# Optimization experiments

Hardware: AMD Instinct MI355X
Metric: run time of the kernel (lower is better)

## Reference

```python
import jax, jax.numpy as jnp
import numpy as np

HEAD = 16  # from init_kwargs
NEG_FILL = -1e20


def setup_inputs() -> dict:
    key = jax.random.key(0)
    ks = jax.random.split(key, 6)
    N, S, E = 4, 2048, 1024
    D = E // HEAD  # 64
    value = jax.random.normal(ks[0], (N, S, E), dtype=jnp.float32)
    key_t = jax.random.normal(ks[1], (N, S, E), dtype=jnp.float32)
    query = jax.random.normal(ks[2], (N, S, E), dtype=jnp.float32)
    # multiplicative causal mask broadcastable to (N, H, S, S)
    mask = jnp.tril(jnp.ones((S, S), dtype=jnp.float32))[None, None, :, :]
    # per-head-dim projection weights (Dense(head_dim) applied after reshape,
    # so weights are (D, D), shared across heads) -- faithful to source
    sc = 1.0 / np.sqrt(D)
    Wq = jax.random.normal(ks[3], (D, D), dtype=jnp.float32) * sc
    Wk = jax.random.normal(ks[4], (D, D), dtype=jnp.float32) * sc
    Wv = jax.random.normal(ks[5], (D, D), dtype=jnp.float32) * sc
    return {"value": value, "key": key_t, "query": query, "mask": mask,
            "Wq": Wq, "Wk": Wk, "Wv": Wv}


def reference(value, key, query, mask, Wq, Wk, Wv):
    N, Lq, E = query.shape
    H = HEAD
    D = E // H
    # reshape to heads, then project last dim (D -> D)
    q = jnp.einsum('nqhd,de->nqhe', query.reshape(N, Lq, H, D), Wq)
    k = jnp.einsum('nkhd,de->nkhe', key.reshape(N, key.shape[1], H, D), Wk)
    v = jnp.einsum('nvhd,de->nvhe', value.reshape(N, value.shape[1], H, D), Wv)
    # unscaled QK^T (source has no 1/sqrt(d))
    energy = jnp.einsum('nqhd,nkhd->nhqk', q, k)  # (N,H,Lq,Lk)
    energy = energy * mask
    energy = jnp.where(energy == 0, NEG_FILL, energy)
    attention = jax.nn.softmax(energy, axis=-1)
    out = jnp.einsum('nhql,nlhd->nqhd', attention, v).reshape(N, Lq, H * D)
    return out  # fc_layer defined in __init__ but never used in call()
```

## Files before the change

kernel.cpp:

```cpp
#include <hip/hip_runtime.h>
#include <hip/hip_bf16.h>
#include <math.h>


#define NB  4
#define SEQ 2048
#define HD  16
#define DH  64
#define NH  (NB*HD)

typedef _Float16 half8  __attribute__((ext_vector_type(8)));
typedef _Float16 half2  __attribute__((ext_vector_type(2)));
typedef __fp16   fp16x2 __attribute__((ext_vector_type(2)));
typedef float    f32x4  __attribute__((ext_vector_type(4)));
typedef float    f32x16 __attribute__((ext_vector_type(16)));

__device__ inline half2 pkrtz(float a, float b) {
  union { fp16x2 f; half2 h; } u;
  u.f = __builtin_amdgcn_cvt_pkrtz(a, b);
  return u.h;
}

__device__ inline void gload16(const void* g, void* l) {
  __builtin_amdgcn_global_load_lds(
      (const __attribute__((address_space(1))) void*)g,
      (__attribute__((address_space(3))) void*)l, 16, 0, 0);
}

__global__ __launch_bounds__(256) void proj_kernel(
    const float* __restrict__ q_in, const float* __restrict__ k_in,
    const float* __restrict__ v_in,
    const float* __restrict__ Wq, const float* __restrict__ Wk,
    const float* __restrict__ Wv,
    _Float16* __restrict__ Qp, _Float16* __restrict__ Kp,
    _Float16* __restrict__ Vt)
{
  __shared__ float Wl[64*64];
  const int t = threadIdx.x;
  const int which = blockIdx.z;
  const float* in = which == 0 ? q_in : (which == 1 ? k_in : v_in);
  const float* W  = which == 0 ? Wq   : (which == 1 ? Wk   : Wv);

  const int nh = blockIdx.y;
  const int n = nh >> 4, h = nh & 15;
  const int s0 = blockIdx.x * 256;

  #pragma unroll
  for (int i = 0; i < 16; ++i) Wl[i*256 + t] = W[i*256 + t];
  __syncthreads();

  const int w = t >> 6, lane = t & 63, lr = lane & 15, lg = lane >> 4;

  if (which < 2) {
    half8 bfr[4][2];
    #pragma unroll
    for (int g = 0; g < 4; ++g)
      #pragma unroll
      for (int kc = 0; kc < 2; ++kc)
        #pragma unroll
        for (int i = 0; i < 8; ++i)
          bfr[g][kc][i] = (_Float16)Wl[(kc*32 + lg*8 + i)*64 + 16*g + lr];

    _Float16* outp = (which == 0 ? Qp : Kp) + (size_t)nh*SEQ*DH;
    #pragma unroll
    for (int pass = 0; pass < 4; ++pass) {
      int row0 = s0 + (pass*4 + w)*16;
      const float* ip = in + ((size_t)(n*SEQ + row0 + lr))*(HD*DH) + h*DH;
      float4 a0 = *(const float4*)(ip + lg*8);
      float4 a1 = *(const float4*)(ip + lg*8 + 4);
      float4 a2 = *(const float4*)(ip + 32 + lg*8);
      float4 a3 = *(const float4*)(ip + 32 + lg*8 + 4);
      half8 af0, af1;
      af0[0]=(_Float16)a0.x; af0[1]=(_Float16)a0.y; af0[2]=(_Float16)a0.z; af0[3]=(_Float16)a0.w;
      af0[4]=(_Float16)a1.x; af0[5]=(_Float16)a1.y; af0[6]=(_Float16)a1.z; af0[7]=(_Float16)a1.w;
      af1[0]=(_Float16)a2.x; af1[1]=(_Float16)a2.y; af1[2]=(_Float16)a2.z; af1[3]=(_Float16)a2.w;
      af1[4]=(_Float16)a3.x; af1[5]=(_Float16)a3.y; af1[6]=(_Float16)a3.z; af1[7]=(_Float16)a3.w;
      f32x4 c[4] = {{0,0,0,0},{0,0,0,0},{0,0,0,0},{0,0,0,0}};
      #pragma unroll
      for (int g = 0; g < 4; ++g) {
        c[g] = __builtin_amdgcn_mfma_f32_16x16x32_f16(af0, bfr[g][0], c[g], 0, 0, 0);
        c[g] = __builtin_amdgcn_mfma_f32_16x16x32_f16(af1, bfr[g][1], c[g], 0, 0, 0);
      }
      #pragma unroll
      for (int g = 0; g < 4; ++g)
        #pragma unroll
        for (int j = 0; j < 4; ++j)
          outp[(size_t)(row0 + 4*lg + j)*DH + 16*g + lr] = (_Float16)c[g][j];
    }
  } else {
    half8 afr[2];
    #pragma unroll
    for (int kc = 0; kc < 2; ++kc)
      #pragma unroll
      for (int i = 0; i < 8; ++i)
        afr[kc][i] = (_Float16)Wl[(kc*32 + lg*8 + i)*64 + w*16 + lr];

    _Float16* outp = Vt + (size_t)nh*DH*SEQ;
    #pragma unroll
    for (int pass = 0; pass < 4; ++pass) {
      int sc0 = s0 + pass*64;
      f32x4 c[4] = {{0,0,0,0},{0,0,0,0},{0,0,0,0},{0,0,0,0}};
      #pragma unroll
      for (int g = 0; g < 4; ++g) {
        const float* ip = in + ((size_t)(n*SEQ + sc0 + 16*g + lr))*(HD*DH) + h*DH;
        float4 b0 = *(const float4*)(ip + lg*8);
        float4 b1 = *(const float4*)(ip + lg*8 + 4);
        float4 b2 = *(const float4*)(ip + 32 + lg*8);
        float4 b3 = *(const float4*)(ip + 32 + lg*8 + 4);
        half8 bf0, bf1;
        bf0[0]=(_Float16)b0.x; bf0[1]=(_Float16)b0.y; bf0[2]=(_Float16)b0.z; bf0[3]=(_Float16)b0.w;
        bf0[4]=(_Float16)b1.x; bf0[5]=(_Float16)b1.y; bf0[6]=(_Float16)b1.z; bf0[7]=(_Float16)b1.w;
        bf1[0]=(_Float16)b2.x; bf1[1]=(_Float16)b2.y; bf1[2]=(_Float16)b2.z; bf1[3]=(_Float16)b2.w;
        bf1[4]=(_Float16)b3.x; bf1[5]=(_Float16)b3.y; bf1[6]=(_Float16)b3.z; bf1[7]=(_Float16)b3.w;
        c[g] = __builtin_amdgcn_mfma_f32_16x16x32_f16(afr[0], bf0, c[g], 0, 0, 0);
        c[g] = __builtin_amdgcn_mfma_f32_16x16x32_f16(afr[1], bf1, c[g], 0, 0, 0);
      }
      #pragma unroll
      for (int g = 0; g < 4; ++g)
        #pragma unroll
        for (int j = 0; j < 4; ++j) {
          int kcol = 16*g + lr;
          int pcol = (kcol & ~12) | ((kcol & 8) >> 1) | ((kcol & 4) << 1);
          outp[(size_t)(w*16 + 4*lg + j)*SEQ + sc0 + pcol] = (_Float16)c[g][j];
        }
    }
  }
}

__global__ __launch_bounds__(256) void attn_kernel(
    const _Float16* __restrict__ Qp,
    const _Float16* __restrict__ Kp,
    const _Float16* __restrict__ Vt,
    float* __restrict__ out)
{
  __shared__ __attribute__((aligned(16))) _Float16 Kl[2][64*64];
  __shared__ __attribute__((aligned(16))) _Float16 Vl[2][64*64];

  const int nh = blockIdx.y;
  const int n = nh >> 4, h = nh & 15;
  const int sb = ((blockIdx.y >> 4) & 1) ? (int)blockIdx.x : (15 - (int)blockIdx.x);
  const int qs = sb * 128;
  const int tid = threadIdx.x;
  const int w = tid >> 6, lane = tid & 63;
  const int lq = lane & 31, lg1 = lane >> 5;
  const int q0 = qs + w*32;
  const int q  = q0 + lq;

  const _Float16* Kbase = Kp + (size_t)nh*SEQ*DH;
  const _Float16* Vbase = Vt + (size_t)nh*DH*SEQ;

  const _Float16* Qrow = Qp + ((size_t)nh*SEQ + q)*DH + 8*lg1;
  half8 qf[4];
  #pragma unroll
  for (int c = 0; c < 4; ++c) qf[c] = *(const half8*)(Qrow + 16*c);

  int roff[2][4];
  #pragma unroll
  for (int rt = 0; rt < 2; ++rt)
    #pragma unroll
    for (int c = 0; c < 4; ++c)
      roff[rt][c] = (32*rt + lq)*128 + (((2*c + lg1) ^ (lq & 7)) << 4);

  const int srow = tid >> 3;
  const int scs  = (tid & 7) ^ (srow & 7);
  const _Float16* kg = Kbase + (size_t)srow*DH + scs*8;
  const _Float16* vg = Vbase + (size_t)srow*SEQ + scs*8;

  float m = -INFINITY, lsum = 0.f;
  f32x16 o0 = {0,0,0,0,0,0,0,0,0,0,0,0,0,0,0,0};
  f32x16 o1 = {0,0,0,0,0,0,0,0,0,0,0,0,0,0,0,0};

  const int Tw   = q0 >> 6;
  const int Tmax = 2*sb + 1;

  gload16(kg,            &Kl[0][tid*8]);
  gload16(kg + 32*DH,    &Kl[0][(256+tid)*8]);
  gload16(vg,            &Vl[0][tid*8]);
  gload16(vg + 32*SEQ,   &Vl[0][(256+tid)*8]);

  int cur = 0;
  for (int t = 0; t <= Tmax; ++t) {
    if (t < Tmax) {
      const _Float16* kgt = kg + (size_t)(t+1)*64*DH;
      const _Float16* vgt = vg + (t+1)*64;
      _Float16* kd = &Kl[cur^1][0];
      _Float16* vd = &Vl[cur^1][0];
      gload16(kgt,          kd + tid*8);
      gload16(kgt + 32*DH,  kd + (256+tid)*8);
      gload16(vgt,          vd + tid*8);
      gload16(vgt + 32*SEQ, vd + (256+tid)*8);
      asm volatile("s_waitcnt vmcnt(4)" ::: "memory");
    } else {
      asm volatile("s_waitcnt vmcnt(0)" ::: "memory");
    }
    __builtin_amdgcn_sched_barrier(0);
    __builtin_amdgcn_s_barrier();
    __builtin_amdgcn_sched_barrier(0);

    if (t <= Tw) {
      const char* Kb = (const char*)&Kl[cur][0];
      const char* Vb = (const char*)&Vl[cur][0];
      const int kt = t*64;

      f32x16 s0 = {0,0,0,0,0,0,0,0,0,0,0,0,0,0,0,0};
      f32x16 s1 = {0,0,0,0,0,0,0,0,0,0,0,0,0,0,0,0};
      #pragma unroll
      for (int c = 0; c < 4; ++c) {
        half8 ka = *(const half8*)(Kb + roff[0][c]);
        half8 kb = *(const half8*)(Kb + roff[1][c]);
        s0 = __builtin_amdgcn_mfma_f32_32x32x16_f16(ka, qf[c], s0, 0, 0, 0);
        s1 = __builtin_amdgcn_mfma_f32_32x32x16_f16(kb, qf[c], s1, 0, 0, 0);
      }
      if (t == Tw) {
        #pragma unroll
        for (int j = 0; j < 16; ++j) {
          int kl = 4*lg1 + 8*(j>>2) + (j&3);
          if (kt + kl      > q) s0[j] = -1e30f;
          if (kt + 32 + kl > q) s1[j] = -1e30f;
        }
      }
      float t0[8];
      #pragma unroll
      for (int j = 0; j < 8; ++j)
        t0[j] = fmaxf(fmaxf(s0[j], s0[j+8]), fmaxf(s1[j], s1[j+8]));
      float pm = fmaxf(fmaxf(fmaxf(t0[0],t0[1]), fmaxf(t0[2],t0[3])),
                       fmaxf(fmaxf(t0[4],t0[5]), fmaxf(t0[6],t0[7])));
      pm = fmaxf(pm, __shfl_xor(pm, 32));
      float mn = fmaxf(m, pm);
      float sc = __expf(m - mn);
      m = mn;
      #pragma unroll
      for (int j = 0; j < 16; ++j) {
        s0[j] = __expf(s0[j] - m);
        s1[j] = __expf(s1[j] - m);
      }
      float u0[8];
      #pragma unroll
      for (int j = 0; j < 8; ++j)
        u0[j] = (s0[j] + s0[j+8]) + (s1[j] + s1[j+8]);
      float ps = ((u0[0]+u0[1]) + (u0[2]+u0[3])) + ((u0[4]+u0[5]) + (u0[6]+u0[7]));
      ps += __shfl_xor(ps, 32);
      lsum = lsum*sc + ps;
      #pragma unroll
      for (int j = 0; j < 16; ++j) { o0[j] *= sc; o1[j] *= sc; }

      half2 pkA[8], pkB[8];
      #pragma unroll
      for (int jj = 0; jj < 8; ++jj) {
        pkA[jj] = pkrtz(s0[2*jj], s0[2*jj+1]);
        pkB[jj] = pkrtz(s1[2*jj], s1[2*jj+1]);
      }
      #pragma unroll
      for (int c = 0; c < 4; ++c) {
        union { half8 h; half2 p[4]; } pb;
        pb.p[0] = (c < 2) ? pkA[(c&1)*4 + 0] : pkB[(c&1)*4 + 0];
        pb.p[1] = (c < 2) ? pkA[(c&1)*4 + 1] : pkB[(c&1)*4 + 1];
        pb.p[2] = (c < 2) ? pkA[(c&1)*4 + 2] : pkB[(c&1)*4 + 2];
        pb.p[3] = (c < 2) ? pkA[(c&1)*4 + 3] : pkB[(c&1)*4 + 3];
        half8 va = *(const half8*)(Vb + roff[0][c]);
        half8 vb = *(const half8*)(Vb + roff[1][c]);
        o0 = __builtin_amdgcn_mfma_f32_32x32x16_f16(va, pb.h, o0, 0, 0, 0);
        o1 = __builtin_amdgcn_mfma_f32_32x32x16_f16(vb, pb.h, o1, 0, 0, 0);
      }
    }

    __builtin_amdgcn_sched_barrier(0);
    __builtin_amdgcn_s_barrier();
    cur ^= 1;
  }

  float inv = 1.0f / lsum;
  float* orow = out + ((size_t)n*SEQ + q)*(HD*DH) + h*DH;
  #pragma unroll
  for (int j = 0; j < 16; ++j) {
    int dl = 4*lg1 + 8*(j>>2) + (j&3);
    orow[dl]      = o0[j] * inv;
    orow[32 + dl] = o1[j] * inv;
  }
}

extern "C" void kernel_launch(void* const* d_in, const int* in_sizes, int n_in,
                              void* d_out, int out_size, void* d_ws, size_t ws_size,
                              hipStream_t stream) {
  (void)in_sizes; (void)n_in; (void)out_size; (void)ws_size;
  const float* value = (const float*)d_in[0];
  const float* key   = (const float*)d_in[1];
  const float* query = (const float*)d_in[2];
  const float* Wq = (const float*)d_in[4];
  const float* Wk = (const float*)d_in[5];
  const float* Wv = (const float*)d_in[6];

  _Float16* Qp = (_Float16*)d_ws;
  _Float16* Kp = Qp + (size_t)NH*SEQ*DH;
  _Float16* Vt = Kp + (size_t)NH*SEQ*DH;
  float* out = (float*)d_out;

  proj_kernel<<<dim3(8, 64, 3), 256, 0, stream>>>(query, key, value,
                                                  Wq, Wk, Wv, Qp, Kp, Vt);
  attn_kernel<<<dim3(16, 64), 256, 0, stream>>>(Qp, Kp, Vt, out);
}
```

Measured before the change: 127.5 us.

## Use single-wave attention blocks with direct global K/V loads, exp2 and lazy rescale

```diff
diff --git a/kernel.cpp b/kernel.cpp
--- a/kernel.cpp
+++ b/kernel.cpp
@@ -19,12 +19,6 @@
   union { fp16x2 f; half2 h; } u;
   u.f = __builtin_amdgcn_cvt_pkrtz(a, b);
   return u.h;
-}
-
-__device__ inline void gload16(const void* g, void* l) {
-  __builtin_amdgcn_global_load_lds(
-      (const __attribute__((address_space(1))) void*)g,
-      (__attribute__((address_space(3))) void*)l, 16, 0, 0);
 }
 
 __global__ __launch_bounds__(256) void proj_kernel(
@@ -52,6 +46,7 @@
   const int w = t >> 6, lane = t & 63, lr = lane & 15, lg = lane >> 4;
 
   if (which < 2) {
+    const float oscale = (which == 0) ? 1.44269504088896f : 1.0f;
     half8 bfr[4][2];
     #pragma unroll
     for (int g = 0; g < 4; ++g)
@@ -85,7 +80,8 @@
       for (int g = 0; g < 4; ++g)
         #pragma unroll
         for (int j = 0; j < 4; ++j)
-          outp[(size_t)(row0 + 4*lg + j)*DH + 16*g + lr] = (_Float16)c[g][j];
+          outp[(size_t)(row0 + 4*lg + j)*DH + 16*g + lr] =
+              (_Float16)(c[g][j] * oscale);
     }
   } else {
     half8 afr[2];
@@ -127,146 +123,102 @@
   }
 }
 
-__global__ __launch_bounds__(256) void attn_kernel(
+__global__ __launch_bounds__(64) void attn_kernel(
     const _Float16* __restrict__ Qp,
     const _Float16* __restrict__ Kp,
     const _Float16* __restrict__ Vt,
     float* __restrict__ out)
 {
-  __shared__ __attribute__((aligned(16))) _Float16 Kl[2][64*64];
-  __shared__ __attribute__((aligned(16))) _Float16 Vl[2][64*64];
-
-  const int nh = blockIdx.y;
-  const int n = nh >> 4, h = nh & 15;
-  const int sb = ((blockIdx.y >> 4) & 1) ? (int)blockIdx.x : (15 - (int)blockIdx.x);
-  const int qs = sb * 128;
-  const int tid = threadIdx.x;
-  const int w = tid >> 6, lane = tid & 63;
+  const int bid  = blockIdx.x;
+  const int head = bid & 63;
+  const int q32  = bid >> 6;
+  const int n = head >> 4, h = head & 15;
+  const int lane = threadIdx.x;
   const int lq = lane & 31, lg1 = lane >> 5;
-  const int q0 = qs + w*32;
+  const int q0 = q32 * 32;
   const int q  = q0 + lq;
-
-  const _Float16* Kbase = Kp + (size_t)nh*SEQ*DH;
-  const _Float16* Vbase = Vt + (size_t)nh*DH*SEQ;
-
-  const _Float16* Qrow = Qp + ((size_t)nh*SEQ + q)*DH + 8*lg1;
+  const int Tmax = q32 >> 1;
+
+  const _Float16* Kbase = Kp + (size_t)head*SEQ*DH;
+  const _Float16* Vbase = Vt + (size_t)head*DH*SEQ;
+
+  const _Float16* Qrow = Qp + ((size_t)head*SEQ + q)*DH + 8*lg1;
   half8 qf[4];
   #pragma unroll
   for (int c = 0; c < 4; ++c) qf[c] = *(const half8*)(Qrow + 16*c);
 
-  int roff[2][4];
-  #pragma unroll
-  for (int rt = 0; rt < 2; ++rt)
-    #pragma unroll
-    for (int c = 0; c < 4; ++c)
-      roff[rt][c] = (32*rt + lq)*128 + (((2*c + lg1) ^ (lq & 7)) << 4);
-
-  const int srow = tid >> 3;
-  const int scs  = (tid & 7) ^ (srow & 7);
-  const _Float16* kg = Kbase + (size_t)srow*DH + scs*8;
-  const _Float16* vg = Vbase + (size_t)srow*SEQ + scs*8;
-
   float m = -INFINITY, lsum = 0.f;
   f32x16 o0 = {0,0,0,0,0,0,0,0,0,0,0,0,0,0,0,0};
   f32x16 o1 = {0,0,0,0,0,0,0,0,0,0,0,0,0,0,0,0};
 
-  const int Tw   = q0 >> 6;
-  const int Tmax = 2*sb + 1;
-
-  gload16(kg,            &Kl[0][tid*8]);
-  gload16(kg + 32*DH,    &Kl[0][(256+tid)*8]);
-  gload16(vg,            &Vl[0][tid*8]);
-  gload16(vg + 32*SEQ,   &Vl[0][(256+tid)*8]);
-
-  int cur = 0;
   for (int t = 0; t <= Tmax; ++t) {
-    if (t < Tmax) {
-      const _Float16* kgt = kg + (size_t)(t+1)*64*DH;
-      const _Float16* vgt = vg + (t+1)*64;
-      _Float16* kd = &Kl[cur^1][0];
-      _Float16* vd = &Vl[cur^1][0];
-      gload16(kgt,          kd + tid*8);
-      gload16(kgt + 32*DH,  kd + (256+tid)*8);
-      gload16(vgt,          vd + tid*8);
-      gload16(vgt + 32*SEQ, vd + (256+tid)*8);
-      asm volatile("s_waitcnt vmcnt(4)" ::: "memory");
-    } else {
-      asm volatile("s_waitcnt vmcnt(0)" ::: "memory");
-    }
-    __builtin_amdgcn_sched_barrier(0);
-    __builtin_amdgcn_s_barrier();
-    __builtin_amdgcn_sched_barrier(0);
-
-    if (t <= Tw) {
-      const char* Kb = (const char*)&Kl[cur][0];
-      const char* Vb = (const char*)&Vl[cur][0];
-      const int kt = t*64;
-
-      f32x16 s0 = {0,0,0,0,0,0,0,0,0,0,0,0,0,0,0,0};
-      f32x16 s1 = {0,0,0,0,0,0,0,0,0,0,0,0,0,0,0,0};
-      #pragma unroll
-      for (int c = 0; c < 4; ++c) {
-        half8 ka = *(const half8*)(Kb + roff[0][c]);
-        half8 kb = *(const half8*)(Kb + roff[1][c]);
-        s0 = __builtin_amdgcn_mfma_f32_32x32x16_f16(ka, qf[c], s0, 0, 0, 0);
-        s1 = __builtin_amdgcn_mfma_f32_32x32x16_f16(kb, qf[c], s1, 0, 0, 0);
+    const int kt = t*64;
+
+    const _Float16* kp = Kbase + (size_t)(kt + lq)*DH + 8*lg1;
+    f32x16 s0 = {0,0,0,0,0,0,0,0,0,0,0,0,0,0,0,0};
+    f32x16 s1 = {0,0,0,0,0,0,0,0,0,0,0,0,0,0,0,0};
+    #pragma unroll
+    for (int c = 0; c < 4; ++c) {
+      half8 ka = *(const half8*)(kp + 16*c);
+      half8 kb = *(const half8*)(kp + 32*DH + 16*c);
+      s0 = __builtin_amdgcn_mfma_f32_32x32x16_f16(ka, qf[c], s0, 0, 0, 0);
+      s1 = __builtin_amdgcn_mfma_f32_32x32x16_f16(kb, qf[c], s1, 0, 0, 0);
+    }
+    if (t == Tmax) {
+      #pragma unroll
+      for (int j = 0; j < 16; ++j) {
+        int kl = 4*lg1 + 8*(j>>2) + (j&3);
+        if (kt + kl      > q) s0[j] = -1e30f;
+        if (kt + 32 + kl > q) s1[j] = -1e30f;
       }
-      if (t == Tw) {
-        #pragma unroll
-        for (int j = 0; j < 16; ++j) {
-          int kl = 4*lg1 + 8*(j>>2) + (j&3);
-          if (kt + kl      > q) s0[j] = -1e30f;
-          if (kt + 32 + kl > q) s1[j] = -1e30f;
-        }
-      }
-      float t0[8];
-      #pragma unroll
-      for (int j = 0; j < 8; ++j)
-        t0[j] = fmaxf(fmaxf(s0[j], s0[j+8]), fmaxf(s1[j], s1[j+8]));
-      float pm = fmaxf(fmaxf(fmaxf(t0[0],t0[1]), fmaxf(t0[2],t0[3])),
-                       fmaxf(fmaxf(t0[4],t0[5]), fmaxf(t0[6],t0[7])));
-      pm = fmaxf(pm, __shfl_xor(pm, 32));
+    }
+    float t0[8];
+    #pragma unroll
+    for (int j = 0; j < 8; ++j)
+      t0[j] = fmaxf(fmaxf(s0[j], s0[j+8]), fmaxf(s1[j], s1[j+8]));
+    float pm = fmaxf(fmaxf(fmaxf(t0[0],t0[1]), fmaxf(t0[2],t0[3])),
+                     fmaxf(fmaxf(t0[4],t0[5]), fmaxf(t0[6],t0[7])));
+    pm = fmaxf(pm, __shfl_xor(pm, 32));
+    if (!__all(pm <= m + 8.f)) {
       float mn = fmaxf(m, pm);
-      float sc = __expf(m - mn);
+      float sc = exp2f(m - mn);
       m = mn;
-      #pragma unroll
-      for (int j = 0; j < 16; ++j) {
-        s0[j] = __expf(s0[j] - m);
-        s1[j] = __expf(s1[j] - m);
-      }
-      float u0[8];
-      #pragma unroll
-      for (int j = 0; j < 8; ++j)
-        u0[j] = (s0[j] + s0[j+8]) + (s1[j] + s1[j+8]);
-      float ps = ((u0[0]+u0[1]) + (u0[2]+u0[3])) + ((u0[4]+u0[5]) + (u0[6]+u0[7]));
-      ps += __shfl_xor(ps, 32);
-      lsum = lsum*sc + ps;
+      lsum *= sc;
       #pragma unroll
       for (int j = 0; j < 16; ++j) { o0[j] *= sc; o1[j] *= sc; }
-
-      half2 pkA[8], pkB[8];
-      #pragma unroll
-      for (int jj = 0; jj < 8; ++jj) {
-        pkA[jj] = pkrtz(s0[2*jj], s0[2*jj+1]);
-        pkB[jj] = pkrtz(s1[2*jj], s1[2*jj+1]);
-      }
-      #pragma unroll
-      for (int c = 0; c < 4; ++c) {
-        union { half8 h; half2 p[4]; } pb;
-        pb.p[0] = (c < 2) ? pkA[(c&1)*4 + 0] : pkB[(c&1)*4 + 0];
-        pb.p[1] = (c < 2) ? pkA[(c&1)*4 + 1] : pkB[(c&1)*4 + 1];
-        pb.p[2] = (c < 2) ? pkA[(c&1)*4 + 2] : pkB[(c&1)*4 + 2];
-        pb.p[3] = (c < 2) ? pkA[(c&1)*4 + 3] : pkB[(c&1)*4 + 3];
-        half8 va = *(const half8*)(Vb + roff[0][c]);
-        half8 vb = *(const half8*)(Vb + roff[1][c]);
-        o0 = __builtin_amdgcn_mfma_f32_32x32x16_f16(va, pb.h, o0, 0, 0, 0);
-        o1 = __builtin_amdgcn_mfma_f32_32x32x16_f16(vb, pb.h, o1, 0, 0, 0);
-      }
-    }
-
-    __builtin_amdgcn_sched_barrier(0);
-    __builtin_amdgcn_s_barrier();
-    cur ^= 1;
+    }
+    #pragma unroll
+    for (int j = 0; j < 16; ++j) {
+      s0[j] = exp2f(s0[j] - m);
+      s1[j] = exp2f(s1[j] - m);
+    }
+    float u0[8];
+    #pragma unroll
+    for (int j = 0; j < 8; ++j)
+      u0[j] = (s0[j] + s0[j+8]) + (s1[j] + s1[j+8]);
+    float ps = ((u0[0]+u0[1]) + (u0[2]+u0[3])) + ((u0[4]+u0[5]) + (u0[6]+u0[7]));
+    ps += __shfl_xor(ps, 32);
+    lsum += ps;
+
+    half2 pkA[8], pkB[8];
+    #pragma unroll
+    for (int jj = 0; jj < 8; ++jj) {
+      pkA[jj] = pkrtz(s0[2*jj], s0[2*jj+1]);
+      pkB[jj] = pkrtz(s1[2*jj], s1[2*jj+1]);
+    }
+    const _Float16* vp = Vbase + (size_t)lq*SEQ + kt + 8*lg1;
+    #pragma unroll
+    for (int c = 0; c < 4; ++c) {
+      union { half8 h; half2 p[4]; } pb;
+      pb.p[0] = (c < 2) ? pkA[(c&1)*4 + 0] : pkB[(c&1)*4 + 0];
+      pb.p[1] = (c < 2) ? pkA[(c&1)*4 + 1] : pkB[(c&1)*4 + 1];
+      pb.p[2] = (c < 2) ? pkA[(c&1)*4 + 2] : pkB[(c&1)*4 + 2];
+      pb.p[3] = (c < 2) ? pkA[(c&1)*4 + 3] : pkB[(c&1)*4 + 3];
+      half8 va = *(const half8*)(vp + 16*c);
+      half8 vb = *(const half8*)(vp + 32*SEQ + 16*c);
+      o0 = __builtin_amdgcn_mfma_f32_32x32x16_f16(va, pb.h, o0, 0, 0, 0);
+      o1 = __builtin_amdgcn_mfma_f32_32x32x16_f16(vb, pb.h, o1, 0, 0, 0);
+    }
   }
 
   float inv = 1.0f / lsum;
@@ -297,5 +249,5 @@
 
   proj_kernel<<<dim3(8, 64, 3), 256, 0, stream>>>(query, key, value,
                                                   Wq, Wk, Wv, Qp, Kp, Vt);
-  attn_kernel<<<dim3(16, 64), 256, 0, stream>>>(Qp, Kp, Vt, out);
-}
+  attn_kernel<<<dim3(4096), 64, 0, stream>>>(Qp, Kp, Vt, out);
+}
```

New measurement: 174.1 us. 36.5% more time.
